# Kernel optimization log

Hardware: AMD Instinct MI355X
Metric: run time of the kernel (lower is better)

## Reference

```python
import jax, jax.numpy as jnp
import numpy as np

V, E_DIM, HID, GNN_O, HEADS = 50257, 256, 128, 128, 4
N_NODES, N_EDGES, T_LEN = 10000, 160000, 64
NEG_SLOPE = 0.2


def gatv2(x, src, dst, Wl, Wr, att, bias, concat):
    """PyG GATv2Conv (share_weights=False, self-loops already in src/dst)."""
    heads, out_ch = att.shape
    n = x.shape[0]
    xl = (x @ Wl).reshape(n, heads, out_ch)   # source transform
    xr = (x @ Wr).reshape(n, heads, out_ch)   # target transform
    e = jax.nn.leaky_relu(xl[src] + xr[dst], NEG_SLOPE)        # [E, h, c]
    logits = jnp.einsum('ehc,hc->eh', e, att)                  # [E, h]
    m = jax.ops.segment_max(logits, dst, num_segments=n)
    a = jnp.exp(logits - m[dst])
    a = a / jax.ops.segment_sum(a, dst, num_segments=n)[dst]
    out = jax.ops.segment_sum(xl[src] * a[..., None], dst, num_segments=n)
    out = out.reshape(n, heads * out_ch) if concat else out.mean(axis=1)
    return out + bias


def setup_inputs() -> dict:
    key = jax.random.key(0)
    ks = jax.random.split(key, 16)
    g = lambda k, shape: jax.random.normal(k, shape, jnp.float32) * 0.05
    x_nodes = jax.random.randint(ks[0], (N_NODES,), 0, V)
    edge_index = jax.random.randint(ks[1], (2, N_EDGES), 0, N_NODES)
    target_sequence = jax.random.randint(ks[2], (1, T_LEN), 0, V)
    return dict(
        x_nodes=x_nodes, edge_index=edge_index, target_sequence=target_sequence,
        embedding=g(ks[3], (V, E_DIM)),
        W1l=g(ks[4], (E_DIM, HEADS * HID)), W1r=g(ks[5], (E_DIM, HEADS * HID)),
        att1=g(ks[6], (HEADS, HID)), b1=jnp.zeros((HEADS * HID,), jnp.float32),
        W2l=g(ks[7], (HEADS * HID, GNN_O)), W2r=g(ks[8], (HEADS * HID, GNN_O)),
        att2=g(ks[9], (1, GNN_O)), b2=jnp.zeros((GNN_O,), jnp.float32),
        Wih=g(ks[10], (3 * HID, GNN_O + E_DIM)), Whh=g(ks[11], (3 * HID, HID)),
        bih=jnp.zeros((3 * HID,), jnp.float32), bhh=jnp.zeros((3 * HID,), jnp.float32),
        Wout=g(ks[12], (V, HID)), bout=jnp.zeros((V,), jnp.float32),
    )


def reference(x_nodes, edge_index, target_sequence, embedding,
              W1l, W1r, att1, b1, W2l, W2r, att2, b2,
              Wih, Whh, bih, bhh, Wout, bout):
    n = x_nodes.shape[0]
    loops = jnp.arange(n, dtype=edge_index.dtype)
    src = jnp.concatenate([edge_index[0], loops])   # add self-loops (PyG default)
    dst = jnp.concatenate([edge_index[1], loops])
    feats = embedding[x_nodes]                      # [N, E_DIM] (dropout off: eval)
    h1 = jax.nn.elu(gatv2(feats, src, dst, W1l, W1r, att1, b1, concat=True))
    enc = gatv2(h1, src, dst, W2l, W2r, att2, b2, concat=False)  # [N, GNN_O]
    context = enc.mean(axis=0)                      # constant across decode steps

    # teacher forcing (ratio=1.0): input tokens are SOS(0) then shifted targets
    tokens = jnp.concatenate([jnp.zeros((1,), target_sequence.dtype),
                              target_sequence[0, :-1]])

    def step(h, tok):
        x = jnp.concatenate([embedding[tok], context])          # [E_DIM+GNN_O]
        gi = Wih @ x + bih
        gh = Whh @ h + bhh
        ir, iz, inn = jnp.split(gi, 3)
        hr, hz, hn = jnp.split(gh, 3)
        r = jax.nn.sigmoid(ir + hr)
        z = jax.nn.sigmoid(iz + hz)
        cand = jnp.tanh(inn + r * hn)
        h_new = (1.0 - z) * cand + z * h
        logits = Wout @ h_new + bout
        return h_new, logits

    h0 = jnp.zeros((Whh.shape[1],), jnp.float32)
    _, logits = jax.lax.scan(step, h0, tokens)      # [T, V]
    return logits[None]                              # [1, T, V]
```

## Files before the change

### kernel.cpp

```cpp
#include <hip/hip_runtime.h>
#include <hip/hip_bf16.h>
#include <math.h>

#define NNODES 10000
#define NEDGES 160000
#define EDIM   256
#define HIDC   128
#define TLEN   64
#define VOCAB  50257
#define NEG    0.2f

typedef __bf16 bf16x8 __attribute__((ext_vector_type(8)));
typedef float  f32x4  __attribute__((ext_vector_type(4)));

static __device__ __forceinline__ float leaky(float x){ return x > 0.f ? x : NEG*x; }
static __device__ __forceinline__ float sigm (float x){ return __fdividef(1.f, 1.f + __expf(-x)); }
static __device__ __forceinline__ float eluf (float x){ return x > 0.f ? x : expm1f(x); }
static __device__ __forceinline__ unsigned short bf16rn(float f){
  unsigned a = __float_as_uint(f);
  return (unsigned short)((a + 0x7FFFu + ((a >> 16) & 1u)) >> 16);
}
static __device__ __forceinline__ float upf(unsigned short u){ return __uint_as_float(((unsigned)u) << 16); }

__global__ void k_featsb(const int* __restrict__ xn, const float* __restrict__ emb,
                         unsigned short* __restrict__ featsb){
  int node = blockIdx.x*4 + (threadIdx.x >> 6);
  int l = threadIdx.x & 63;
  float4 v = ((const float4*)(emb + (size_t)xn[node]*EDIM))[l];
  ushort4 o; o.x = bf16rn(v.x); o.y = bf16rn(v.y); o.z = bf16rn(v.z); o.w = bf16rn(v.w);
  *(ushort4*)(featsb + (size_t)node*EDIM + 4*l) = o;
}

__global__ void k_wcast(const float* __restrict__ in, unsigned short* __restrict__ out, int n4){
  int idx = blockIdx.x*256 + threadIdx.x;
  if (idx < n4){
    float4 v = ((const float4*)in)[idx];
    ushort4 o; o.x = bf16rn(v.x); o.y = bf16rn(v.y); o.z = bf16rn(v.z); o.w = bf16rn(v.w);
    ((ushort4*)out)[idx] = o;
  }
}

__global__ __launch_bounds__(256) void k_tr(const float* __restrict__ in,
    unsigned short* __restrict__ out, int K, int Nin)
{
  __shared__ unsigned short tile[64][72];
  int k0 = blockIdx.x*64, n0 = blockIdx.y*64;
  int t = threadIdx.x;
  int tr = t >> 4, tc4 = (t & 15)*4;
  #pragma unroll
  for (int it = 0; it < 4; ++it){
    int kr = tr + 16*it;
    float4 v = *(const float4*)(in + (size_t)(k0+kr)*Nin + n0 + tc4);
    tile[tc4+0][kr] = bf16rn(v.x);
    tile[tc4+1][kr] = bf16rn(v.y);
    tile[tc4+2][kr] = bf16rn(v.z);
    tile[tc4+3][kr] = bf16rn(v.w);
  }
  __syncthreads();
  #pragma unroll
  for (int it = 0; it < 4; ++it){
    int nr = tr + 16*it;
    ushort4 o;
    o.x = tile[nr][tc4+0]; o.y = tile[nr][tc4+1];
    o.z = tile[nr][tc4+2]; o.w = tile[nr][tc4+3];
    *(ushort4*)(out + (size_t)(n0+nr)*K + k0 + tc4) = o;
  }
}

__global__ void k_deg(const int* __restrict__ dst, int* __restrict__ deg){
  int e = blockIdx.x*256 + threadIdx.x;
  if (e < NEDGES) atomicAdd(&deg[dst[e]], 1);
}

__global__ __launch_bounds__(1024) void k_scan(const int* __restrict__ deg, int* __restrict__ offs){
  __shared__ int s[1024];
  int t = threadIdx.x;
  int loc[10]; int sum = 0;
  #pragma unroll
  for (int q = 0; q < 10; q++){
    int idx = t*10 + q;
    loc[q] = sum;
    sum += (idx < NNODES) ? deg[idx] : 0;
  }
  s[t] = sum;
  __syncthreads();
  for (int ofs = 1; ofs < 1024; ofs <<= 1){
    int v = (t >= ofs) ? s[t-ofs] : 0;
    __syncthreads();
    s[t] += v;
    __syncthreads();
  }
  int pre = (t > 0) ? s[t-1] : 0;
  #pragma unroll
  for (int q = 0; q < 10; q++){
    int idx = t*10 + q;
    if (idx < NNODES) offs[idx] = pre + loc[q];
  }
  if (t == 1023) offs[NNODES] = s[1023];
}

__global__ void k_scatter(const int* __restrict__ src, const int* __restrict__ dst,
                          const int* __restrict__ offs, int* __restrict__ cursor,
                          int* __restrict__ esrc){
  int e = blockIdx.x*256 + threadIdx.x;
  if (e >= NEDGES) return;
  int d = dst[e];
  int p = atomicAdd(&cursor[d], 1);
  esrc[offs[d] + p] = src[e];
}

template<int KDIM>
__global__ __launch_bounds__(256) void k_mfma(const unsigned short* __restrict__ A,
    const unsigned short* __restrict__ Bt, unsigned short* __restrict__ C,
    int M, int N)
{
  __shared__ __align__(16) unsigned short As[128*64];
  __shared__ __align__(16) unsigned short Bs[128*64];
  int tid = threadIdx.x;
  int l   = tid & 63;
  int wid = tid >> 6;
  int wr = wid >> 1, wc = wid & 1;
  int row0 = blockIdx.x * 128, col0 = blockIdx.y * 128;
  int lr = l & 15, kg = l >> 4;
  f32x4 acc[4][4] = {};

  for (int kt = 0; kt < KDIM/64; ++kt){
    int k0 = kt*64;
    #pragma unroll
    for (int c = 0; c < 4; ++c){
      int chunk = wid*4 + c;
      int arow = row0 + chunk*8 + (l >> 3);
      if (arow > M-1) arow = M-1;
      const unsigned short* ga = A + (size_t)arow*KDIM + k0 + (l & 7)*8;
      __builtin_amdgcn_global_load_lds(
          (const __attribute__((address_space(1))) void*)ga,
          (__attribute__((address_space(3))) void*)(As + chunk*512), 16, 0, 0);
      int brow = col0 + chunk*8 + (l >> 3);
      const unsigned short* gb = Bt + (size_t)brow*KDIM + k0 + (l & 7)*8;
      __builtin_amdgcn_global_load_lds(
          (const __attribute__((address_space(1))) void*)gb,
          (__attribute__((address_space(3))) void*)(Bs + chunk*512), 16, 0, 0);
    }
    __syncthreads();
    #pragma unroll
    for (int ks = 0; ks < 2; ++ks){
      bf16x8 af[4], bfr[4];
      #pragma unroll
      for (int m = 0; m < 4; ++m)
        af[m] = *(const bf16x8*)(As + (wr*64 + m*16 + lr)*64 + ks*32 + kg*8);
      #pragma unroll
      for (int n = 0; n < 4; ++n)
        bfr[n] = *(const bf16x8*)(Bs + (wc*64 + n*16 + lr)*64 + ks*32 + kg*8);
      #pragma unroll
      for (int m = 0; m < 4; ++m)
        #pragma unroll
        for (int n = 0; n < 4; ++n)
          acc[m][n] = __builtin_amdgcn_mfma_f32_16x16x32_bf16(af[m], bfr[n], acc[m][n], 0, 0, 0);
    }
    __syncthreads();
  }

  #pragma unroll
  for (int m = 0; m < 4; ++m){
    int rbase = row0 + wr*64 + m*16 + kg*4;
    #pragma unroll
    for (int r = 0; r < 4; ++r){
      int row = rbase + r;
      if (row < M){
        #pragma unroll
        for (int n = 0; n < 4; ++n){
          int col = col0 + wc*64 + n*16 + lr;
          C[(size_t)row*N + col] = bf16rn(acc[m][n][r]);
        }
      }
    }
  }
}

__global__ __launch_bounds__(256) void k_mout(const unsigned short* __restrict__ A,
    const unsigned short* __restrict__ Bt, const float* __restrict__ bias,
    float* __restrict__ out)
{
  __shared__ __align__(16) unsigned short As[64*128];
  __shared__ __align__(16) unsigned short Bs[128*128];
  int tid = threadIdx.x;
  int l   = tid & 63;
  int wid = tid >> 6;
  int col0 = blockIdx.x * 128;
  int lr = l & 15, kg = l >> 4;

  #pragma unroll
  for (int c = 0; c < 4; ++c){
    int chunk = wid*4 + c;
    const unsigned short* ga = A + (size_t)(chunk*4 + (l >> 4))*128 + (l & 15)*8;
    __builtin_amdgcn_global_load_lds(
        (const __attribute__((address_space(1))) void*)ga,
        (__attribute__((address_space(3))) void*)(As + chunk*512), 16, 0, 0);
  }
  #pragma unroll
  for (int c = 0; c < 8; ++c){
    int chunk = wid*8 + c;
    int brow = col0 + chunk*4 + (l >> 4);
    if (brow > VOCAB-1) brow = VOCAB-1;
    const unsigned short* gb = Bt + (size_t)brow*128 + (l & 15)*8;
    __builtin_amdgcn_global_load_lds(
        (const __attribute__((address_space(1))) void*)gb,
        (__attribute__((address_space(3))) void*)(Bs + chunk*512), 16, 0, 0);
  }
  __syncthreads();

  f32x4 acc[4][2] = {};
  #pragma unroll
  for (int ks = 0; ks < 4; ++ks){
    bf16x8 af[4], bfr[2];
    #pragma unroll
    for (int m = 0; m < 4; ++m)
      af[m] = *(const bf16x8*)(As + (m*16 + lr)*128 + ks*32 + kg*8);
    #pragma unroll
    for (int n = 0; n < 2; ++n)
      bfr[n] = *(const bf16x8*)(Bs + (wid*32 + n*16 + lr)*128 + ks*32 + kg*8);
    #pragma unroll
    for (int m = 0; m < 4; ++m)
      #pragma unroll
      for (int n = 0; n < 2; ++n)
        acc[m][n] = __builtin_amdgcn_mfma_f32_16x16x32_bf16(af[m], bfr[n], acc[m][n], 0, 0, 0);
  }

  #pragma unroll
  for (int n = 0; n < 2; ++n){
    int col = col0 + wid*32 + n*16 + lr;
    if (col < VOCAB){
      float bv = bias[col];
      #pragma unroll
      for (int m = 0; m < 4; ++m){
        #pragma unroll
        for (int r = 0; r < 4; ++r){
          int trow = m*16 + kg*4 + r;
          out[(size_t)trow*VOCAB + col] = acc[m][n][r] + bv;
        }
      }
    }
  }
}

__global__ __launch_bounds__(256) void k_gat1(const unsigned short* __restrict__ xlr,
    const int* __restrict__ esrc, const int* __restrict__ offs,
    const float* __restrict__ att, const float* __restrict__ b1,
    unsigned short* __restrict__ h1b)
{
  int node = blockIdx.x*4 + (threadIdx.x >> 6);
  int l = threadIdx.x & 63;
  const unsigned short* bi = xlr + (size_t)node*1024;
  ushort4 u;
  u = *(const ushort4*)(bi + 512 + 4*l);
  float4 xr1; xr1.x = upf(u.x); xr1.y = upf(u.y); xr1.z = upf(u.z); xr1.w = upf(u.w);
  u = *(const ushort4*)(bi + 768 + 4*l);
  float4 xr2; xr2.x = upf(u.x); xr2.y = upf(u.y); xr2.z = upf(u.z); xr2.w = upf(u.w);
  int hq = l >> 5;
  float4 at1 = *(const float4*)(att + hq*HIDC + ((4*l) & 127));
  float4 at2 = *(const float4*)(att + (2+hq)*HIDC + ((4*l) & 127));
  float4 ac1 = {0,0,0,0}, ac2 = {0,0,0,0};
  float d1 = 0.f, d2 = 0.f;
  int beg = offs[node], end = offs[node+1];
  for (int p = beg-1; p < end; ++p){
    int s = (p < beg) ? node : esrc[p];
    const unsigned short* bs = xlr + (size_t)s*1024;
    ushort4 u1 = *(const ushort4*)(bs + 4*l);
    ushort4 u2 = *(const ushort4*)(bs + 256 + 4*l);
    float4 x1; x1.x = upf(u1.x); x1.y = upf(u1.y); x1.z = upf(u1.z); x1.w = upf(u1.w);
    float4 x2; x2.x = upf(u2.x); x2.y = upf(u2.y); x2.z = upf(u2.z); x2.w = upf(u2.w);
    float p1 = leaky(x1.x+xr1.x)*at1.x + leaky(x1.y+xr1.y)*at1.y
             + leaky(x1.z+xr1.z)*at1.z + leaky(x1.w+xr1.w)*at1.w;
    float p2 = leaky(x2.x+xr2.x)*at2.x + leaky(x2.y+xr2.y)*at2.y
             + leaky(x2.z+xr2.z)*at2.z + leaky(x2.w+xr2.w)*at2.w;
    #pragma unroll
    for (int m = 1; m <= 16; m <<= 1){
      p1 += __shfl_xor(p1, m);
      p2 += __shfl_xor(p2, m);
    }
    float w1 = __expf(p1), w2 = __expf(p2);
    ac1.x = fmaf(w1, x1.x, ac1.x); ac1.y = fmaf(w1, x1.y, ac1.y);
    ac1.z = fmaf(w1, x1.z, ac1.z); ac1.w = fmaf(w1, x1.w, ac1.w);
    ac2.x = fmaf(w2, x2.x, ac2.x); ac2.y = fmaf(w2, x2.y, ac2.y);
    ac2.z = fmaf(w2, x2.z, ac2.z); ac2.w = fmaf(w2, x2.w, ac2.w);
    d1 += w1; d2 += w2;
  }
  float i1 = 1.f/d1, i2 = 1.f/d2;
  const float* bq1 = b1 + 4*l;
  const float* bq2 = b1 + 256 + 4*l;
  ushort4 o1, o2;
  o1.x = bf16rn(eluf(ac1.x*i1 + bq1[0])); o1.y = bf16rn(eluf(ac1.y*i1 + bq1[1]));
  o1.z = bf16rn(eluf(ac1.z*i1 + bq1[2])); o1.w = bf16rn(eluf(ac1.w*i1 + bq1[3]));
  o2.x = bf16rn(eluf(ac2.x*i2 + bq2[0])); o2.y = bf16rn(eluf(ac2.y*i2 + bq2[1]));
  o2.z = bf16rn(eluf(ac2.z*i2 + bq2[2])); o2.w = bf16rn(eluf(ac2.w*i2 + bq2[3]));
  *(ushort4*)(h1b + (size_t)node*512 + 4*l)       = o1;
  *(ushort4*)(h1b + (size_t)node*512 + 256 + 4*l) = o2;
}

__global__ __launch_bounds__(256) void k_gat2(const unsigned short* __restrict__ xlr2,
    const int* __restrict__ esrc, const int* __restrict__ offs,
    const float* __restrict__ att2, const float* __restrict__ b2,
    float* __restrict__ enc)
{
  int node = blockIdx.x*4 + (threadIdx.x >> 6);
  int l = threadIdx.x & 63;
  const unsigned short* bi = xlr2 + (size_t)node*256;
  ushort2 v = *(const ushort2*)(bi + 128 + 2*l);
  float2 xr; xr.x = upf(v.x); xr.y = upf(v.y);
  float2 at = *(const float2*)(att2 + 2*l);
  float2 ac = {0,0}; float den = 0.f;
  int beg = offs[node], end = offs[node+1];
  for (int p = beg-1; p < end; ++p){
    int s = (p < beg) ? node : esrc[p];
    ushort2 xv = *(const ushort2*)(xlr2 + (size_t)s*256 + 2*l);
    float2 x; x.x = upf(xv.x); x.y = upf(xv.y);
    float pp = leaky(x.x+xr.x)*at.x + leaky(x.y+xr.y)*at.y;
    #pragma unroll
    for (int m = 1; m <= 32; m <<= 1) pp += __shfl_xor(pp, m);
    float w = __expf(pp);
    ac.x = fmaf(w, x.x, ac.x); ac.y = fmaf(w, x.y, ac.y);
    den += w;
  }
  float inv = 1.f/den;
  float2 o; o.x = ac.x*inv + b2[2*l]; o.y = ac.y*inv + b2[2*l+1];
  *(float2*)(enc + (size_t)node*128 + 2*l) = o;
}

__global__ void k_mean(const float* __restrict__ enc, float* __restrict__ ctx){
  int c = threadIdx.x & 127;
  int slice = blockIdx.x*2 + (threadIdx.x >> 7);
  float s = 0.f;
  for (int i = slice; i < NNODES; i += 160) s += enc[(size_t)i*128 + c];
  atomicAdd(&ctx[c], s * (1.f/NNODES));
}

__global__ __launch_bounds__(384) void k_gi(const int* __restrict__ tseq,
    const float* __restrict__ emb, const float* __restrict__ ctx,
    const float* __restrict__ Wih, const float* __restrict__ bih,
    float* __restrict__ Gi)
{
  __shared__ float xs[384];
  int t = blockIdx.x, tid = threadIdx.x;
  int tok = (t == 0) ? 0 : tseq[t-1];
  if (tid < 256) xs[tid] = emb[(size_t)tok*EDIM + tid];
  else           xs[tid] = ctx[tid - 256];
  __syncthreads();
  const float* w = Wih + (size_t)tid*384;
  float acc = bih[tid];
  #pragma unroll 8
  for (int k = 0; k < 384; k++) acc = fmaf(w[k], xs[k], acc);
  Gi[t*384 + tid] = acc;
}

__global__ __launch_bounds__(384) void k_gru(const float* __restrict__ Gi,
    const float* __restrict__ Whh, const float* __restrict__ bhh,
    unsigned short* __restrict__ HTt)
{
  __shared__ float GH[384];
  __shared__ alignas(16) float HS[128];
  int tid = threadIdx.x;
  float w[128];
  {
    const float4* wrow = (const float4*)(Whh + (size_t)tid*HIDC);
    #pragma unroll
    for (int k = 0; k < 32; k++){
      float4 v = wrow[k];
      w[4*k+0] = v.x; w[4*k+1] = v.y; w[4*k+2] = v.z; w[4*k+3] = v.w;
    }
  }
  float bh = bhh[tid];
  float hloc = 0.f;
  if (tid < 128) HS[tid] = 0.f;
  __syncthreads();

  const float4* H4 = (const float4*)HS;

  for (int t = 0; t < TLEN; t++){
    float gi0 = 0.f, gi1 = 0.f, gi2 = 0.f;
    if (tid < 128){
      gi0 = Gi[t*384 + tid];
      gi1 = Gi[t*384 + 128 + tid];
      gi2 = Gi[t*384 + 256 + tid];
    }
    float a0 = 0.f, a1 = 0.f, a2 = 0.f, a3 = 0.f;
    #pragma unroll
    for (int q = 0; q < 16; q++){
      float4 ha = H4[2*q];
      float4 hb = H4[2*q+1];
      a0 = fmaf(w[8*q+0], ha.x, a0);
      a1 = fmaf(w[8*q+1], ha.y, a1);
      a2 = fmaf(w[8*q+2], ha.z, a2);
      a3 = fmaf(w[8*q+3], ha.w, a3);
      a0 = fmaf(w[8*q+4], hb.x, a0);
      a1 = fmaf(w[8*q+5], hb.y, a1);
      a2 = fmaf(w[8*q+6], hb.z, a2);
      a3 = fmaf(w[8*q+7], hb.w, a3);
    }
    float acc = ((a0 + a1) + (a2 + a3)) + bh;
    if (tid >= 128) GH[tid] = acc;
    __syncthreads();
    if (tid < 128){
      float gr = gi0 + acc;
      float gz = gi1 + GH[128 + tid];
      float hn = GH[256 + tid];
      float r = sigm(gr);
      float z = sigm(gz);
      float e2 = __expf(2.f*(gi2 + r*hn));
      float cand = __fdividef(e2 - 1.f, e2 + 1.f);
      float hnew = (1.f - z)*cand + z*hloc;
      hloc = hnew;
      HS[tid] = hnew;
      HTt[t*HIDC + tid] = bf16rn(hnew);
    }
    __syncthreads();
  }
}

extern "C" void kernel_launch(void* const* d_in, const int* in_sizes, int n_in,
                              void* d_out, int out_size, void* d_ws, size_t ws_size,
                              hipStream_t stream)
{
  const int*   x_nodes = (const int*)  d_in[0];
  const int*   eidx    = (const int*)  d_in[1];
  const int*   tseq    = (const int*)  d_in[2];
  const float* emb     = (const float*)d_in[3];
  const float* W1l     = (const float*)d_in[4];
  const float* W1r     = (const float*)d_in[5];
  const float* att1    = (const float*)d_in[6];
  const float* b1      = (const float*)d_in[7];
  const float* W2l     = (const float*)d_in[8];
  const float* W2r     = (const float*)d_in[9];
  const float* att2    = (const float*)d_in[10];
  const float* b2      = (const float*)d_in[11];
  const float* Wih     = (const float*)d_in[12];
  const float* Whh     = (const float*)d_in[13];
  const float* bih     = (const float*)d_in[14];
  const float* bhh     = (const float*)d_in[15];
  const float* Wout    = (const float*)d_in[16];
  const float* bout    = (const float*)d_in[17];
  float* out = (float*)d_out;
  char*  ws  = (char*)d_ws;

  unsigned short* xlr1b  = (unsigned short*)(ws);
  unsigned short* h1b    = (unsigned short*)(ws + 20480000);
  unsigned short* featsb = (unsigned short*)(ws + 30720000);
  unsigned short* xlr2b  = (unsigned short*)(ws + 35840000);
  float*          enc    = (float*)        (ws + 40960000);
  unsigned short* Bt1    = (unsigned short*)(ws + 46080000);
  unsigned short* Bt2    = (unsigned short*)(ws + 46604288);
  int*   deg    = (int*)(ws + 46866432);
  int*   offs   = (int*)(ws + 46906432);
  int*   cursor = (int*)(ws + 46946436);
  int*   esrc   = (int*)(ws + 46986436);
  float* ctx    = (float*)(ws + 47626440);
  float* Gi     = (float*)(ws + 47627008);
  unsigned short* HTt   = (unsigned short*)(ws + 47725312);
  unsigned short* Woutb = (unsigned short*)(ws + 47741696);

  hipMemsetAsync(deg,    0, NNODES*sizeof(int), stream);
  hipMemsetAsync(cursor, 0, NNODES*sizeof(int), stream);

  k_featsb<<<2500, 256, 0, stream>>>(x_nodes, emb, featsb);
  k_wcast <<<6283, 256, 0, stream>>>(Wout, Woutb, VOCAB*128/4);
  k_tr<<<dim3(4,8), 256, 0, stream>>>(W1l, Bt1,            256, 512);
  k_tr<<<dim3(4,8), 256, 0, stream>>>(W1r, Bt1 + 512*256,  256, 512);
  k_tr<<<dim3(8,2), 256, 0, stream>>>(W2l, Bt2,            512, 128);
  k_tr<<<dim3(8,2), 256, 0, stream>>>(W2r, Bt2 + 128*512,  512, 128);

  k_deg    <<<625, 256, 0, stream>>>(eidx + NEDGES, deg);
  k_scan   <<<1,  1024, 0, stream>>>(deg, offs);
  k_scatter<<<625, 256, 0, stream>>>(eidx, eidx + NEDGES, offs, cursor, esrc);

  k_mfma<256><<<dim3(79,8), 256, 0, stream>>>(featsb, Bt1, xlr1b, NNODES, 1024);
  k_gat1<<<2500, 256, 0, stream>>>(xlr1b, esrc, offs, att1, b1, h1b);

  k_mfma<512><<<dim3(79,2), 256, 0, stream>>>(h1b, Bt2, xlr2b, NNODES, 256);
  k_gat2<<<2500, 256, 0, stream>>>(xlr2b, esrc, offs, att2, b2, enc);

  hipMemsetAsync(ctx, 0, 128*sizeof(float), stream);
  k_mean<<<80, 256, 0, stream>>>(enc, ctx);
  k_gi  <<<TLEN, 384, 0, stream>>>(tseq, emb, ctx, Wih, bih, Gi);
  k_gru <<<1, 384, 0, stream>>>(Gi, Whh, bhh, HTt);

  k_mout<<<393, 256, 0, stream>>>(HTt, Woutb, bout, out);
}
```

Before: 286.9 us.

## Compute GRU recurrent matvec with MFMA using split bf16 hidden state

Replaces the per-thread fp32 register dot product in the sequential GRU kernel with MFMA 16x16x32 bf16 instructions. Whh is held in registers as bf16 fragments, and the hidden state is split into hi and lo bf16 parts to keep precision. The intent is to shorten each of the 64 serial steps. In exchange, Whh is rounded to bf16, which adds error, and only one column of each MFMA output is used.

```diff
diff --git a/kernel.cpp b/kernel.cpp
--- a/kernel.cpp
+++ b/kernel.cpp
@@ -12,6 +12,7 @@
 
 typedef __bf16 bf16x8 __attribute__((ext_vector_type(8)));
 typedef float  f32x4  __attribute__((ext_vector_type(4)));
+typedef unsigned short u16x8 __attribute__((ext_vector_type(8)));
 
 static __device__ __forceinline__ float leaky(float x){ return x > 0.f ? x : NEG*x; }
 static __device__ __forceinline__ float sigm (float x){ return __fdividef(1.f, 1.f + __expf(-x)); }
@@ -357,23 +358,37 @@
     unsigned short* __restrict__ HTt)
 {
   __shared__ float GH[384];
-  __shared__ alignas(16) float HS[128];
+  __shared__ __align__(16) unsigned short hhi[128];
+  __shared__ __align__(16) unsigned short hlo[128];
   int tid = threadIdx.x;
-  float w[128];
-  {
-    const float4* wrow = (const float4*)(Whh + (size_t)tid*HIDC);
-    #pragma unroll
-    for (int k = 0; k < 32; k++){
-      float4 v = wrow[k];
-      w[4*k+0] = v.x; w[4*k+1] = v.y; w[4*k+2] = v.z; w[4*k+3] = v.w;
-    }
-  }
-  float bh = bhh[tid];
-  float hloc = 0.f;
-  if (tid < 128) HS[tid] = 0.f;
+  int l = tid & 63, w = tid >> 6;
+  int lr = l & 15, kg = l >> 4;
+
+  bf16x8 afr[4][4];
+  #pragma unroll
+  for (int t4 = 0; t4 < 4; ++t4){
+    int row = w*64 + t4*16 + lr;
+    const float* rp = Whh + (size_t)row*HIDC;
+    #pragma unroll
+    for (int ks = 0; ks < 4; ++ks){
+      const float* p = rp + ks*32 + kg*8;
+      float4 v0 = *(const float4*)p;
+      float4 v1 = *(const float4*)(p + 4);
+      u16x8 u;
+      u[0] = bf16rn(v0.x); u[1] = bf16rn(v0.y); u[2] = bf16rn(v0.z); u[3] = bf16rn(v0.w);
+      u[4] = bf16rn(v1.x); u[5] = bf16rn(v1.y); u[6] = bf16rn(v1.z); u[7] = bf16rn(v1.w);
+      afr[t4][ks] = __builtin_bit_cast(bf16x8, u);
+    }
+  }
+
+  float bh0 = 0.f, bh1 = 0.f, bh2 = 0.f, hloc = 0.f;
+  if (tid < 128){
+    bh0 = bhh[tid];
+    bh1 = bhh[128 + tid];
+    bh2 = bhh[256 + tid];
+    hhi[tid] = 0; hlo[tid] = 0;
+  }
   __syncthreads();
-
-  const float4* H4 = (const float4*)HS;
 
   for (int t = 0; t < TLEN; t++){
     float gi0 = 0.f, gi1 = 0.f, gi2 = 0.f;
@@ -382,35 +397,42 @@
       gi1 = Gi[t*384 + 128 + tid];
       gi2 = Gi[t*384 + 256 + tid];
     }
-    float a0 = 0.f, a1 = 0.f, a2 = 0.f, a3 = 0.f;
-    #pragma unroll
-    for (int q = 0; q < 16; q++){
-      float4 ha = H4[2*q];
-      float4 hb = H4[2*q+1];
-      a0 = fmaf(w[8*q+0], ha.x, a0);
-      a1 = fmaf(w[8*q+1], ha.y, a1);
-      a2 = fmaf(w[8*q+2], ha.z, a2);
-      a3 = fmaf(w[8*q+3], ha.w, a3);
-      a0 = fmaf(w[8*q+4], hb.x, a0);
-      a1 = fmaf(w[8*q+5], hb.y, a1);
-      a2 = fmaf(w[8*q+6], hb.z, a2);
-      a3 = fmaf(w[8*q+7], hb.w, a3);
-    }
-    float acc = ((a0 + a1) + (a2 + a3)) + bh;
-    if (tid >= 128) GH[tid] = acc;
+    bf16x8 bhi[4], blo[4];
+    #pragma unroll
+    for (int ks = 0; ks < 4; ++ks){
+      bhi[ks] = *(const bf16x8*)(hhi + ks*32 + kg*8);
+      blo[ks] = *(const bf16x8*)(hlo + ks*32 + kg*8);
+    }
+    f32x4 acc[4] = {};
+    #pragma unroll
+    for (int ks = 0; ks < 4; ++ks){
+      #pragma unroll
+      for (int t4 = 0; t4 < 4; ++t4){
+        acc[t4] = __builtin_amdgcn_mfma_f32_16x16x32_bf16(afr[t4][ks], bhi[ks], acc[t4], 0, 0, 0);
+        acc[t4] = __builtin_amdgcn_mfma_f32_16x16x32_bf16(afr[t4][ks], blo[ks], acc[t4], 0, 0, 0);
+      }
+    }
+    if (lr == 0){
+      #pragma unroll
+      for (int t4 = 0; t4 < 4; ++t4){
+        *(f32x4*)&GH[w*64 + t4*16 + kg*4] = acc[t4];
+      }
+    }
     __syncthreads();
     if (tid < 128){
-      float gr = gi0 + acc;
-      float gz = gi1 + GH[128 + tid];
-      float hn = GH[256 + tid];
+      float gr = gi0 + GH[tid]       + bh0;
+      float gz = gi1 + GH[128 + tid] + bh1;
+      float hn = GH[256 + tid]       + bh2;
       float r = sigm(gr);
       float z = sigm(gz);
       float e2 = __expf(2.f*(gi2 + r*hn));
       float cand = __fdividef(e2 - 1.f, e2 + 1.f);
       float hnew = (1.f - z)*cand + z*hloc;
       hloc = hnew;
-      HS[tid] = hnew;
-      HTt[t*HIDC + tid] = bf16rn(hnew);
+      unsigned short hi = bf16rn(hnew);
+      hhi[tid] = hi;
+      hlo[tid] = bf16rn(hnew - upf(hi));
+      HTt[t*HIDC + tid] = hi;
     }
     __syncthreads();
   }
```

New measurement: 289.2 us. Within noise of the previous version (+0.8%).
